# Performance work log

Measured on AMD Instinct MI355X. Metric: run time of the kernel, lower is better.

## Reference

```python
import jax, jax.numpy as jnp
import numpy as np

IN_FEATURES = 4096
OUT_FEATURES = 2048
N_GROUPS = 16  # group size = IN_FEATURES // N_GROUPS = 256


def setup_inputs() -> dict:
    key = jax.random.key(0)
    k1, k2, k3, k4 = jax.random.split(key, 4)
    x = jax.random.normal(k1, (8, 64, IN_FEATURES), dtype=jnp.float32)
    # uint8 quantized weights, stored [out, in] as in the torch module
    qweight = jax.random.randint(k2, (OUT_FEATURES, IN_FEATURES), 0, 256).astype(jnp.uint8)
    # per-(out-channel, group) dequant scale and offset; scale ~ (max-min)/255 of rand weights
    qrange = jax.random.uniform(k3, (OUT_FEATURES, N_GROUPS), dtype=jnp.float32) * (2.0 / 255.0)
    qmin = -jax.random.uniform(k4, (OUT_FEATURES, N_GROUPS), dtype=jnp.float32)
    return {"x": x, "qweight": qweight, "qrange": qrange, "qmin": qmin}


def reference(x, qweight, qrange, qmin):
    # out[b,s,o] = sum_i x[b,s,i] * (q[o,i]*qrange[o,g(i)] + qmin[o,g(i)])
    B, S, IN = x.shape
    OUT, G = qrange.shape
    gs = IN // G
    xg = x.reshape(B, S, G, gs)                     # [B,S,G,gs]
    qg = qweight.reshape(OUT, G, gs).astype(x.dtype)  # [O,G,gs]
    # fused per-group dequant matmul: scale folded into the contraction
    out = jnp.einsum('bsgi,ogi,og->bso', xg, qg, qrange)
    # offset term: qmin[o,g] * sum_i_in_group x[b,s,i]
    out = out + jnp.einsum('bsg,og->bso', xg.sum(axis=-1), qmin)
    return out
```

## Files before the change

### kernel.cpp

```cpp
#include <hip/hip_runtime.h>
#include <hip/hip_bf16.h>


#define M_T 512
#define N_T 2048
#define K_T 4096
#define NGRP 16
#define BM 128
#define BN 128
#define BK 64
#define OUT_ELEMS (M_T * N_T)
#define W_ELEMS (N_T * K_T)
#define X_ELEMS (M_T * K_T)

typedef __attribute__((ext_vector_type(8))) short mfrag_t;
typedef __attribute__((ext_vector_type(8))) unsigned short u16x8;
typedef __attribute__((ext_vector_type(4))) float f32x4;

__device__ __forceinline__ unsigned short f2bf(float f) {
  union { __hip_bfloat16 h; unsigned short u; } c;
  c.h = __float2bfloat16(f);
  return c.u;
}

__global__ __launch_bounds__(256) void pack_kernel(
    const float* __restrict__ x, const int* __restrict__ qw,
    const float* __restrict__ qrange, const float* __restrict__ qmin,
    unsigned short* __restrict__ wsW, unsigned short* __restrict__ wsX) {
  const int bid = blockIdx.x;
  const int tid = threadIdx.x;
  if (bid < (W_ELEMS / 8) / 256) {
    const int gidx = bid * 256 + tid;
    const int o = gidx >> 9;
    const int k8 = gidx & 511;
    const int g = k8 >> 5;
    const float sc = qrange[o * NGRP + g];
    const float mn = qmin[o * NGRP + g];
    const int4* q = (const int4*)(qw + ((size_t)o << 12) + (k8 << 3));
    const int4 q0 = q[0], q1 = q[1];
    u16x8 p;
    p[0] = f2bf((float)q0.x * sc + mn); p[1] = f2bf((float)q0.y * sc + mn);
    p[2] = f2bf((float)q0.z * sc + mn); p[3] = f2bf((float)q0.w * sc + mn);
    p[4] = f2bf((float)q1.x * sc + mn); p[5] = f2bf((float)q1.y * sc + mn);
    p[6] = f2bf((float)q1.z * sc + mn); p[7] = f2bf((float)q1.w * sc + mn);
    *(u16x8*)(wsW + ((size_t)gidx << 3)) = p;
  } else {
    const int gidx = (bid - (W_ELEMS / 8) / 256) * 256 + tid;
    const float4* a = (const float4*)(x + ((size_t)gidx << 3));
    const float4 a0 = a[0], a1 = a[1];
    u16x8 p;
    p[0] = f2bf(a0.x); p[1] = f2bf(a0.y); p[2] = f2bf(a0.z); p[3] = f2bf(a0.w);
    p[4] = f2bf(a1.x); p[5] = f2bf(a1.y); p[6] = f2bf(a1.z); p[7] = f2bf(a1.w);
    *(u16x8*)(wsX + ((size_t)gidx << 3)) = p;
  }
}

template <int KSPLIT, bool XCDSWZ>
__global__ __launch_bounds__(512, 4) void dq_gemm_kernel(
    const unsigned short* __restrict__ wsX, const unsigned short* __restrict__ wsW,
    float* __restrict__ dst) {
  constexpr int KC = K_T / KSPLIT;
  constexpr int NTC = KC / BK;

  __shared__ __align__(16) unsigned short As[BM * BK];
  __shared__ __align__(16) unsigned short Bs[BN * BK];

  const int tid = threadIdx.x;
  int xt, yt, kc;
  if (XCDSWZ) {
    const int b = blockIdx.x;
    kc = b & 7;
    const int slot = b >> 3;
    xt = slot & 15;
    yt = slot >> 4;
  } else {
    const int b = blockIdx.x;
    xt = b & 15;
    yt = (b >> 4) & 3;
    kc = b >> 6;
  }
  const int n0 = xt * BN;
  const int m0 = yt * BM;
  const int kbase = kc * KC;

  const int srow = tid >> 2;
  const int sseg = tid & 3;

  const unsigned short* ap = wsX + (size_t)(m0 + srow) * K_T + kbase + sseg * 16;
  const unsigned short* bp = wsW + (size_t)(n0 + srow) * K_T + kbase + sseg * 16;

  const int lane = tid & 63;
  const int wv = tid >> 6;
  const int wm = (wv >> 2) * 64;
  const int wn = (wv & 3) * 32;
  const int lr = lane & 15;
  const int lq = lane >> 4;

  const int rx7 = srow & 7;
  const int abase = srow * BK;
  const int wslot0 = ((sseg * 2) ^ rx7) << 3;
  const int wslot1 = ((sseg * 2 + 1) ^ rx7) << 3;
  const int rxl = lr & 7;

  u16x8 av0, av1, bv0, bv1;

  {
    av0 = *(const u16x8*)(ap);
    av1 = *(const u16x8*)(ap + 8);
    bv0 = *(const u16x8*)(bp);
    bv1 = *(const u16x8*)(bp + 8);
  }

  f32x4 acc[4][2] = {};

  for (int t = 0; t < NTC; ++t) {
    if (t > 0) __syncthreads();

    *(u16x8*)&As[abase + wslot0] = av0;
    *(u16x8*)&As[abase + wslot1] = av1;
    *(u16x8*)&Bs[abase + wslot0] = bv0;
    *(u16x8*)&Bs[abase + wslot1] = bv1;

    if (t + 1 < NTC) {
      const unsigned short* a_ = ap + (size_t)(t + 1) * BK;
      const unsigned short* b_ = bp + (size_t)(t + 1) * BK;
      av0 = *(const u16x8*)(a_);
      av1 = *(const u16x8*)(a_ + 8);
      bv0 = *(const u16x8*)(b_);
      bv1 = *(const u16x8*)(b_ + 8);
    }

    __syncthreads();

#pragma unroll
    for (int kk = 0; kk < 2; ++kk) {
      const int so = ((kk * 4 + lq) ^ rxl) << 3;
      mfrag_t af[4], bf[2];
#pragma unroll
      for (int fm = 0; fm < 4; ++fm)
        af[fm] = *(const mfrag_t*)&As[(wm + fm * 16 + lr) * BK + so];
#pragma unroll
      for (int fn = 0; fn < 2; ++fn)
        bf[fn] = *(const mfrag_t*)&Bs[(wn + fn * 16 + lr) * BK + so];
#pragma unroll
      for (int fm = 0; fm < 4; ++fm)
#pragma unroll
        for (int fn = 0; fn < 2; ++fn)
          acc[fm][fn] = __builtin_amdgcn_mfma_f32_16x16x32_bf16(af[fm], bf[fn], acc[fm][fn], 0, 0, 0);
    }
  }

  float* base = dst + (size_t)kc * OUT_ELEMS;
#pragma unroll
  for (int fm = 0; fm < 4; ++fm) {
#pragma unroll
    for (int fn = 0; fn < 2; ++fn) {
      const int r0 = m0 + wm + fm * 16 + lq * 4;
      const int c = n0 + wn + fn * 16 + lr;
      float* op = base + (size_t)r0 * N_T + c;
      op[0 * (size_t)N_T] = acc[fm][fn][0];
      op[1 * (size_t)N_T] = acc[fm][fn][1];
      op[2 * (size_t)N_T] = acc[fm][fn][2];
      op[3 * (size_t)N_T] = acc[fm][fn][3];
    }
  }
}

template <int KSPLIT>
__global__ __launch_bounds__(256) void reduce_kernel(const float* __restrict__ ws,
                                                     float* __restrict__ out) {
  const int i4 = blockIdx.x * 256 + threadIdx.x;
  const size_t base = (size_t)i4 * 4;
  float4 a = *(const float4*)(ws + base);
#pragma unroll
  for (int s = 1; s < KSPLIT; ++s) {
    float4 b = *(const float4*)(ws + (size_t)s * OUT_ELEMS + base);
    a.x += b.x; a.y += b.y; a.z += b.z; a.w += b.w;
  }
  *(float4*)(out + base) = a;
}

__global__ void naive_kernel(const float* __restrict__ x, const int* __restrict__ qw,
                             const float* __restrict__ qrange, const float* __restrict__ qmin,
                             float* __restrict__ out) {
  const int idx = blockIdx.x * 256 + threadIdx.x;
  if (idx >= OUT_ELEMS) return;
  const int m = idx / N_T, n = idx % N_T;
  float s = 0.f;
  for (int g = 0; g < NGRP; ++g) {
    const float sc = qrange[n * NGRP + g], mn = qmin[n * NGRP + g];
    float d = 0.f, xs = 0.f;
    for (int k = g * 256; k < (g + 1) * 256; ++k) {
      d += x[(size_t)m * K_T + k] * (float)qw[(size_t)n * K_T + k];
      xs += x[(size_t)m * K_T + k];
    }
    s += d * sc + xs * mn;
  }
  out[idx] = s;
}

extern "C" void kernel_launch(void* const* d_in, const int* in_sizes, int n_in,
                              void* d_out, int out_size, void* d_ws, size_t ws_size,
                              hipStream_t stream) {
  const float* x = (const float*)d_in[0];
  const int* qw = (const int*)d_in[1];
  const float* qr = (const float*)d_in[2];
  const float* qm = (const float*)d_in[3];
  float* out = (float*)d_out;

  constexpr int KS = 8;
  unsigned short* wsW = (unsigned short*)d_ws;
  unsigned short* wsX = wsW + W_ELEMS;
  float* partials = (float*)(wsX + X_ELEMS);
  const size_t need = (size_t)W_ELEMS * 2 + (size_t)X_ELEMS * 2 +
                      (size_t)KS * OUT_ELEMS * sizeof(float);
  if (ws_size >= need) {
    const int packblk = (W_ELEMS / 8) / 256 + (X_ELEMS / 8) / 256;
    pack_kernel<<<packblk, 256, 0, stream>>>(x, qw, qr, qm, wsW, wsX);
    const int nblk = (N_T / BN) * (M_T / BM) * KS;
    dq_gemm_kernel<KS, true><<<nblk, dim3(512, 1, 1), 0, stream>>>(wsX, wsW, partials);
    reduce_kernel<KS><<<OUT_ELEMS / 4 / 256, 256, 0, stream>>>(partials, out);
  } else {
    naive_kernel<<<(OUT_ELEMS + 255) / 256, 256, 0, stream>>>(x, qw, qr, qm, out);
  }
}
```

Baseline: 35.55 us.

## Stage GEMM tiles with direct global-to-LDS loads instead of register staging

The dequant GEMM now fills its A and B shared-memory tiles with global_load_lds builtins, which write straight into LDS, instead of loading into registers and storing them. The XOR swizzle moves into the global source address so the LDS layout matches the existing fragment reads. This removes the VGPR round trip and the LDS store instructions. The trade-off is that the next tile is only issued after the current tile's compute and a barrier, so the register prefetch overlap is lost and latency hiding falls to other resident waves.

```diff
diff --git a/kernel.cpp b/kernel.cpp
--- a/kernel.cpp
+++ b/kernel.cpp
@@ -83,53 +83,47 @@
   const int m0 = yt * BM;
   const int kbase = kc * KC;
 
-  const int srow = tid >> 2;
-  const int sseg = tid & 3;
-
-  const unsigned short* ap = wsX + (size_t)(m0 + srow) * K_T + kbase + sseg * 16;
-  const unsigned short* bp = wsW + (size_t)(n0 + srow) * K_T + kbase + sseg * 16;
-
   const int lane = tid & 63;
   const int wv = tid >> 6;
   const int wm = (wv >> 2) * 64;
   const int wn = (wv & 3) * 32;
   const int lr = lane & 15;
   const int lq = lane >> 4;
-
-  const int rx7 = srow & 7;
-  const int abase = srow * BK;
-  const int wslot0 = ((sseg * 2) ^ rx7) << 3;
-  const int wslot1 = ((sseg * 2 + 1) ^ rx7) << 3;
   const int rxl = lr & 7;
 
-  u16x8 av0, av1, bv0, bv1;
-
-  {
-    av0 = *(const u16x8*)(ap);
-    av1 = *(const u16x8*)(ap + 8);
-    bv0 = *(const u16x8*)(bp);
-    bv1 = *(const u16x8*)(bp + 8);
-  }
+  const int swzcol = (((lane & 7) ^ (lane >> 3)) << 3);
+  const int r0 = wv * 16 + (lane >> 3);
+  const int r1 = r0 + 8;
+  const unsigned short* gA0 = wsX + (size_t)(m0 + r0) * K_T + kbase + swzcol;
+  const unsigned short* gA1 = wsX + (size_t)(m0 + r1) * K_T + kbase + swzcol;
+  const unsigned short* gB0 = wsW + (size_t)(n0 + r0) * K_T + kbase + swzcol;
+  const unsigned short* gB1 = wsW + (size_t)(n0 + r1) * K_T + kbase + swzcol;
+  unsigned short* lA0 = &As[wv * 1024];
+  unsigned short* lA1 = &As[wv * 1024 + 512];
+  unsigned short* lB0 = &Bs[wv * 1024];
+  unsigned short* lB1 = &Bs[wv * 1024 + 512];
+
+#define STAGE(T)                                                              \
+  do {                                                                        \
+    const size_t o_ = (size_t)(T) * BK;                                       \
+    __builtin_amdgcn_global_load_lds(                                         \
+        (const __attribute__((address_space(1))) void*)(gA0 + o_),            \
+        (__attribute__((address_space(3))) void*)lA0, 16, 0, 0);              \
+    __builtin_amdgcn_global_load_lds(                                         \
+        (const __attribute__((address_space(1))) void*)(gA1 + o_),            \
+        (__attribute__((address_space(3))) void*)lA1, 16, 0, 0);              \
+    __builtin_amdgcn_global_load_lds(                                         \
+        (const __attribute__((address_space(1))) void*)(gB0 + o_),            \
+        (__attribute__((address_space(3))) void*)lB0, 16, 0, 0);              \
+    __builtin_amdgcn_global_load_lds(                                         \
+        (const __attribute__((address_space(1))) void*)(gB1 + o_),            \
+        (__attribute__((address_space(3))) void*)lB1, 16, 0, 0);              \
+  } while (0)
 
   f32x4 acc[4][2] = {};
 
+  STAGE(0);
   for (int t = 0; t < NTC; ++t) {
-    if (t > 0) __syncthreads();
-
-    *(u16x8*)&As[abase + wslot0] = av0;
-    *(u16x8*)&As[abase + wslot1] = av1;
-    *(u16x8*)&Bs[abase + wslot0] = bv0;
-    *(u16x8*)&Bs[abase + wslot1] = bv1;
-
-    if (t + 1 < NTC) {
-      const unsigned short* a_ = ap + (size_t)(t + 1) * BK;
-      const unsigned short* b_ = bp + (size_t)(t + 1) * BK;
-      av0 = *(const u16x8*)(a_);
-      av1 = *(const u16x8*)(a_ + 8);
-      bv0 = *(const u16x8*)(b_);
-      bv1 = *(const u16x8*)(b_ + 8);
-    }
-
     __syncthreads();
 
 #pragma unroll
@@ -148,16 +142,22 @@
         for (int fn = 0; fn < 2; ++fn)
           acc[fm][fn] = __builtin_amdgcn_mfma_f32_16x16x32_bf16(af[fm], bf[fn], acc[fm][fn], 0, 0, 0);
     }
-  }
+
+    if (t + 1 < NTC) {
+      __syncthreads();
+      STAGE(t + 1);
+    }
+  }
+#undef STAGE
 
   float* base = dst + (size_t)kc * OUT_ELEMS;
 #pragma unroll
   for (int fm = 0; fm < 4; ++fm) {
 #pragma unroll
     for (int fn = 0; fn < 2; ++fn) {
-      const int r0 = m0 + wm + fm * 16 + lq * 4;
+      const int rr = m0 + wm + fm * 16 + lq * 4;
       const int c = n0 + wn + fn * 16 + lr;
-      float* op = base + (size_t)r0 * N_T + c;
+      float* op = base + (size_t)rr * N_T + c;
       op[0 * (size_t)N_T] = acc[fm][fn][0];
       op[1 * (size_t)N_T] = acc[fm][fn][1];
       op[2 * (size_t)N_T] = acc[fm][fn][2];
```

After: 35.44 us. Within noise of the previous version (-0.3%).
